# Kernel tuning notes

Measured on AMD Instinct MI355X. Metric: run time of the kernel, lower is better.

The kernel has to match this reference:

```python
import jax, jax.numpy as jnp
import numpy as np

B, C, H, W = 2, 256, 64, 64
NH, HD, K = 4, 64, 16  # num_head, head_channel, n_clusters
N = H * W
SCALE = HD ** 0.5


def _lin(x, Wm, b):
    return x @ Wm + b


def _mlp(x, W1, b1, W2, b2):
    h = _lin(x, W1, b1)
    h = jnp.where(h > 0, h, 0.01 * h)  # LeakyReLU(0.01)
    return _lin(h, W2, b2)  # dropout p=0.0 -> identity


def setup_inputs() -> dict:
    key = jax.random.key(0)
    ks = jax.random.split(key, 20)
    s = 1.0 / np.sqrt(C)
    s2 = 1.0 / np.sqrt(2 * C)
    inp = {
        "q_img": jax.random.normal(ks[0], (B, C, H, W), jnp.float32),
        "k_img_map": jax.random.normal(ks[1], (B, C, H, W), jnp.float32),
        "v_img_map": jax.random.normal(ks[2], (B, C, H, W), jnp.float32),
        "labels": jax.random.randint(ks[3], (B, H, W), 0, K),
        "pixel_coefficients": jax.random.uniform(ks[4], (B, N, N), jnp.float32),
        "Wq": jax.random.uniform(ks[5], (C, C), jnp.float32, -s, s),
        "bq": jnp.zeros((C,), jnp.float32),
        "Wk": jax.random.uniform(ks[6], (C, C), jnp.float32, -s, s),
        "bk": jnp.zeros((C,), jnp.float32),
        "Wv": jax.random.uniform(ks[7], (C, C), jnp.float32, -s, s),
        "bv": jnp.zeros((C,), jnp.float32),
        "W11": jax.random.uniform(ks[8], (C, 2 * C), jnp.float32, -s, s),
        "b11": jnp.zeros((2 * C,), jnp.float32),
        "W12": jax.random.uniform(ks[9], (2 * C, C), jnp.float32, -s2, s2),
        "b12": jnp.zeros((C,), jnp.float32),
        "W21": jax.random.uniform(ks[10], (C, 2 * C), jnp.float32, -s, s),
        "b21": jnp.zeros((2 * C,), jnp.float32),
        "W22": jax.random.uniform(ks[11], (2 * C, C), jnp.float32, -s2, s2),
        "b22": jnp.zeros((C,), jnp.float32),
    }
    return inp


def reference(q_img, k_img_map, v_img_map, labels, pixel_coefficients,
              Wq, bq, Wk, bk, Wv, bv, W11, b11, W12, b12, W21, b21, W22, b22):
    # [B,C,H,W] -> [B,N,C]
    q = _lin(q_img.transpose(0, 2, 3, 1).reshape(B, N, C), Wq, bq)
    k = _lin(k_img_map.transpose(0, 2, 3, 1).reshape(B, N, C), Wk, bk)
    v = _lin(v_img_map.transpose(0, 2, 3, 1).reshape(B, N, C), Wv, bv)

    lab = labels.reshape(B, N)
    onehot = (lab[:, :, None] == jnp.arange(K)[None, None, :]).astype(jnp.float32)  # [B,N,K]
    num_k = jnp.einsum('bnk,bnc->bkc', onehot, k)
    den_k = onehot.sum(axis=1)[:, :, None] + 1e-6
    centers_k = num_k / den_k  # [B,K,C]

    qm = q.reshape(B, N, NH, HD).transpose(0, 2, 1, 3)  # [B,h,N,d]
    km = k.reshape(B, N, NH, HD).transpose(0, 2, 1, 3)
    vm = v.reshape(B, N, NH, HD).transpose(0, 2, 1, 3)
    cm = centers_k.reshape(B, K, NH, HD).transpose(0, 2, 1, 3)  # [B,h,K,d]

    attn_intra = jnp.einsum('bhnd,bhmd->bhnm', qm, km)          # [B,h,N,N]
    attn_centers = jnp.einsum('bhnd,bhkd->bhnk', qm, cm)        # [B,h,N,K]

    same = (lab[:, :, None] == lab[:, None, :])[:, None]        # [B,1,N,N]
    idx = jnp.broadcast_to(lab[:, None, None, :], (B, NH, N, N))
    attn_inter = jnp.take_along_axis(attn_centers, idx, axis=-1) * pixel_coefficients[:, None]

    scores = jnp.where(same, attn_intra, attn_inter) / SCALE
    attn = jax.nn.softmax(scores, axis=-1)
    out = jnp.einsum('bhnm,bhmd->bhnd', attn, vm).transpose(0, 2, 1, 3).reshape(B, N, C)

    rs1 = v + _mlp(out, W11, b11, W12, b12)        # [B,N,C] (v_spatial residual)
    rs2 = rs1 + _mlp(rs1, W21, b21, W22, b22)
    return rs2.reshape(B, H, W, C).transpose(0, 3, 1, 2)  # [B,C,H,W]
```

## Files before the change

kernel.cpp:

```cpp
#include <hip/hip_runtime.h>
#include <stdint.h>

#define Bv 2
#define Cv 256
#define Nv 4096
#define NHv 4
#define HDv 64
#define Kv 16


typedef __attribute__((ext_vector_type(8))) short bf16x8;
typedef __attribute__((ext_vector_type(4))) float f32x4;

__device__ __forceinline__ float bf2f(unsigned short u) {
  union { unsigned int i; float f; } x; x.i = ((unsigned int)u) << 16; return x.f;
}
__device__ __forceinline__ unsigned short f2bf(float f) {
  union { float f; unsigned int i; } x; x.f = f;
  unsigned int r = x.i + 0x7FFF + ((x.i >> 16) & 1);
  return (unsigned short)(r >> 16);
}

__global__ __launch_bounds__(256) void imgt_k(
    const float* __restrict__ qi, const float* __restrict__ ki,
    const float* __restrict__ vi, unsigned short* __restrict__ dst)
{
  const int z = blockIdx.z;
  const float* src = (z < 2 ? qi : (z < 4 ? ki : vi)) + (long long)(z & 1) * Cv * Nv;
  unsigned short* out = dst + (long long)z * Nv * Cv;
  __shared__ float t[32][33];
  const int x = threadIdx.x, y = threadIdx.y;
  const int n0 = blockIdx.x * 32, c0 = blockIdx.y * 32;
  for (int i = y; i < 32; i += 8)
    t[i][x] = src[(long long)(c0 + i) * Nv + n0 + x];
  __syncthreads();
  for (int i = y; i < 32; i += 8)
    out[(long long)(n0 + i) * Cv + c0 + x] = f2bf(t[x][i]);
}

struct WP { const float* p[7]; };

__global__ __launch_bounds__(256) void wt_k(WP wp, unsigned short* __restrict__ dst)
{
  const int z = blockIdx.z;
  const int KD[7] = {256, 256, 256, 256, 512, 256, 512};
  const int ND[7] = {256, 256, 256, 512, 256, 512, 256};
  const long long OFF[7] = {0, 65536, 131072, 196608, 327680, 458752, 589824};
  const int Kw = KD[z], Nw = ND[z];
  const int nb = blockIdx.x * 32, kb2 = blockIdx.y * 32;
  if (nb >= Nw || kb2 >= Kw) return;
  __shared__ float t[32][33];
  const int x = threadIdx.x, y = threadIdx.y;
  const float* src = wp.p[z];
  for (int i = y; i < 32; i += 8)
    t[i][x] = src[(long long)(kb2 + i) * Nw + nb + x];
  __syncthreads();
  for (int i = y; i < 32; i += 8)
    dst[OFF[z] + (long long)(nb + i) * Kw + kb2 + x] = f2bf(t[x][i]);
}

__global__ __launch_bounds__(256) void proj_k(
    const unsigned short* __restrict__ imgT, const unsigned short* __restrict__ wt,
    const float* __restrict__ bq, const float* __restrict__ bk, const float* __restrict__ bv,
    unsigned short* __restrict__ qbf, unsigned short* __restrict__ kbf,
    float* __restrict__ vpp, unsigned short* __restrict__ vtb)
{
  __shared__ __align__(16) unsigned short As[128][72];
  __shared__ __align__(16) unsigned short Bs[128][72];
  const int tid = threadIdx.x;
  const int w = tid >> 6, lane = tid & 63;
  const int lr = lane & 15, quad = lane >> 4;
  const int m0 = blockIdx.x * 128, n0 = blockIdx.y * 128;
  const int z = blockIdx.z, zz = z >> 1, bb = z & 1;
  const int wm = (w >> 1) * 64, wn = (w & 1) * 64;
  const int sr = tid >> 1, sh = (tid & 1) * 32;
  const long long NvCv = (long long)Nv * Cv;

  const float* bias = zz == 0 ? bq : (zz == 1 ? bk : bv);
  const unsigned short* Ab0 = imgT + (long long)z * NvCv + (long long)(m0 + sr) * Cv + sh;
  const unsigned short* Bb0 = wt + (long long)zz * 65536 + (long long)(n0 + sr) * Cv + sh;

  f32x4 acc[4][4];
#pragma unroll
  for (int i = 0; i < 4; ++i)
#pragma unroll
    for (int j = 0; j < 4; ++j) acc[i][j] = (f32x4){0.f, 0.f, 0.f, 0.f};

  for (int k0 = 0; k0 < Cv; k0 += 64) {
    const unsigned short* Ab = Ab0 + k0;
    const unsigned short* Bp = Bb0 + k0;
    uint4 a0 = *(const uint4*)Ab, a1 = *(const uint4*)(Ab + 8);
    uint4 a2 = *(const uint4*)(Ab + 16), a3 = *(const uint4*)(Ab + 24);
    uint4 b0 = *(const uint4*)Bp, b1 = *(const uint4*)(Bp + 8);
    uint4 b2 = *(const uint4*)(Bp + 16), b3 = *(const uint4*)(Bp + 24);
    *(uint4*)&As[sr][sh] = a0; *(uint4*)&As[sr][sh + 8] = a1;
    *(uint4*)&As[sr][sh + 16] = a2; *(uint4*)&As[sr][sh + 24] = a3;
    *(uint4*)&Bs[sr][sh] = b0; *(uint4*)&Bs[sr][sh + 8] = b1;
    *(uint4*)&Bs[sr][sh + 16] = b2; *(uint4*)&Bs[sr][sh + 24] = b3;
    __syncthreads();
#pragma unroll
    for (int ks = 0; ks < 2; ++ks) {
      bf16x8 af[4], bfr[4];
#pragma unroll
      for (int i = 0; i < 4; ++i)
        af[i] = *(const bf16x8*)&As[wm + i * 16 + lr][ks * 32 + quad * 8];
#pragma unroll
      for (int j = 0; j < 4; ++j)
        bfr[j] = *(const bf16x8*)&Bs[wn + j * 16 + lr][ks * 32 + quad * 8];
#pragma unroll
      for (int i = 0; i < 4; ++i)
#pragma unroll
        for (int j = 0; j < 4; ++j)
          acc[i][j] = __builtin_amdgcn_mfma_f32_16x16x32_bf16(af[i], bfr[j], acc[i][j], 0, 0, 0);
    }
    __syncthreads();
  }

#pragma unroll
  for (int j = 0; j < 4; ++j) {
    const int col = n0 + wn + j * 16 + lr;
    const float bvv = bias[col];
#pragma unroll
    for (int i = 0; i < 4; ++i) {
      const int mb = m0 + wm + i * 16 + quad * 4;
      float r[4];
#pragma unroll
      for (int reg = 0; reg < 4; ++reg) r[reg] = acc[i][j][reg] + bvv;
      const long long ob = (long long)bb * NvCv;
      if (zz == 0) {
#pragma unroll
        for (int reg = 0; reg < 4; ++reg)
          qbf[ob + (long long)(mb + reg) * Cv + col] = f2bf(r[reg] * 0.125f);
      } else if (zz == 1) {
#pragma unroll
        for (int reg = 0; reg < 4; ++reg)
          kbf[ob + (long long)(mb + reg) * Cv + col] = f2bf(r[reg]);
      } else {
#pragma unroll
        for (int reg = 0; reg < 4; ++reg)
          vpp[ob + (long long)(mb + reg) * Cv + col] = r[reg];
        uint2 pk;
        pk.x = f2bf(r[0]) | ((unsigned int)f2bf(r[1]) << 16);
        pk.y = f2bf(r[2]) | ((unsigned int)f2bf(r[3]) << 16);
        *(uint2*)&vtb[ob + (long long)col * Nv + mb] = pk;
      }
    }
  }
}

template<bool ABF16, int ACT, int RES, int OM>
__global__ __launch_bounds__(256) void mm_k(
    const void* __restrict__ A, const unsigned short* __restrict__ Bt,
    const float* __restrict__ bias, const float* __restrict__ Res,
    float* __restrict__ outF, unsigned short* __restrict__ outB,
    int M, int Nn, int Kd)
{
  __shared__ __align__(16) unsigned short As[128][72];
  __shared__ __align__(16) unsigned short Bs[128][72];
  const int tid = threadIdx.x;
  const int w = tid >> 6, lane = tid & 63;
  const int lr = lane & 15, quad = lane >> 4;
  const int m0 = blockIdx.x * 128, n0 = blockIdx.y * 128;
  const int wm = (w >> 1) * 64, wn = (w & 1) * 64;
  const int sr = tid >> 1, sh = (tid & 1) * 32;

  f32x4 acc[4][4];
#pragma unroll
  for (int i = 0; i < 4; ++i)
#pragma unroll
    for (int j = 0; j < 4; ++j) acc[i][j] = (f32x4){0.f, 0.f, 0.f, 0.f};

  const long long abase = (long long)(m0 + sr) * Kd + sh;
  const unsigned short* Bb = Bt + (long long)(n0 + sr) * Kd + sh;

  for (int k0 = 0; k0 < Kd; k0 += 64) {
    if (ABF16) {
      const unsigned short* Ab = (const unsigned short*)A + abase + k0;
      uint4 u0 = *(const uint4*)Ab, u1 = *(const uint4*)(Ab + 8);
      uint4 u2 = *(const uint4*)(Ab + 16), u3 = *(const uint4*)(Ab + 24);
      *(uint4*)&As[sr][sh] = u0; *(uint4*)&As[sr][sh + 8] = u1;
      *(uint4*)&As[sr][sh + 16] = u2; *(uint4*)&As[sr][sh + 24] = u3;
    } else {
      const float* Af = (const float*)A + abase + k0;
#pragma unroll
      for (int t = 0; t < 4; ++t) {
        const float4 f0 = *(const float4*)(Af + t * 8);
        const float4 f1 = *(const float4*)(Af + t * 8 + 4);
        uint4 pk;
        pk.x = f2bf(f0.x) | ((unsigned int)f2bf(f0.y) << 16);
        pk.y = f2bf(f0.z) | ((unsigned int)f2bf(f0.w) << 16);
        pk.z = f2bf(f1.x) | ((unsigned int)f2bf(f1.y) << 16);
        pk.w = f2bf(f1.z) | ((unsigned int)f2bf(f1.w) << 16);
        *(uint4*)&As[sr][sh + t * 8] = pk;
      }
    }
    {
      const unsigned short* Bp = Bb + k0;
      uint4 u0 = *(const uint4*)Bp, u1 = *(const uint4*)(Bp + 8);
      uint4 u2 = *(const uint4*)(Bp + 16), u3 = *(const uint4*)(Bp + 24);
      *(uint4*)&Bs[sr][sh] = u0; *(uint4*)&Bs[sr][sh + 8] = u1;
      *(uint4*)&Bs[sr][sh + 16] = u2; *(uint4*)&Bs[sr][sh + 24] = u3;
    }
    __syncthreads();
#pragma unroll
    for (int ks = 0; ks < 2; ++ks) {
      bf16x8 af[4], bfr[4];
#pragma unroll
      for (int i = 0; i < 4; ++i)
        af[i] = *(const bf16x8*)&As[wm + i * 16 + lr][ks * 32 + quad * 8];
#pragma unroll
      for (int j = 0; j < 4; ++j)
        bfr[j] = *(const bf16x8*)&Bs[wn + j * 16 + lr][ks * 32 + quad * 8];
#pragma unroll
      for (int i = 0; i < 4; ++i)
#pragma unroll
        for (int j = 0; j < 4; ++j)
          acc[i][j] = __builtin_amdgcn_mfma_f32_16x16x32_bf16(af[i], bfr[j], acc[i][j], 0, 0, 0);
    }
    __syncthreads();
  }

#pragma unroll
  for (int j = 0; j < 4; ++j) {
    const int col = n0 + wn + j * 16 + lr;
    const float bv = bias[col];
#pragma unroll
    for (int i = 0; i < 4; ++i) {
      const int mb = m0 + wm + i * 16 + quad * 4;
      float r[4];
#pragma unroll
      for (int reg = 0; reg < 4; ++reg) {
        float v = acc[i][j][reg] + bv;
        if (ACT) v = v > 0.f ? v : 0.01f * v;
        if (RES) v += Res[(long long)(mb + reg) * Nn + col];
        r[reg] = v;
      }
      if (OM == 0) {
#pragma unroll
        for (int reg = 0; reg < 4; ++reg)
          outF[(long long)(mb + reg) * Nn + col] = r[reg];
      } else if (OM == 1) {
#pragma unroll
        for (int reg = 0; reg < 4; ++reg)
          outB[(long long)(mb + reg) * Nn + col] = f2bf(r[reg]);
      } else {
        const float4 st = {r[0], r[1], r[2], r[3]};
        *(float4*)&outF[((long long)((mb >> 12) * Cv + col)) * Nv + (mb & 4095)] = st;
      }
    }
  }
}

__global__ __launch_bounds__(256) void zero_k(float* p, int n)
{
  const int i = blockIdx.x * 256 + threadIdx.x;
  if (i < n) p[i] = 0.f;
}

__global__ __launch_bounds__(256) void center_accum(
    const unsigned short* __restrict__ kb, const int* __restrict__ labels,
    float* __restrict__ cent, float* __restrict__ cnts)
{
  __shared__ int lab_s[512];
  const int bx = blockIdx.x;
  const int chunk = bx & 7;
  const int kk = (bx >> 3) & 15;
  const int b = bx >> 7;
  const int c = threadIdx.x;
  const int nbase = chunk * 512;
  for (int i = threadIdx.x; i < 512; i += 256) lab_s[i] = labels[b * Nv + nbase + i];
  __syncthreads();
  float acc = 0.f;
  int cnt = 0;
#pragma unroll 4
  for (int i = 0; i < 512; ++i) {
    if (lab_s[i] == kk) {
      acc += bf2f(kb[(long long)(b * Nv + nbase + i) * Cv + c]);
      ++cnt;
    }
  }
  atomicAdd(&cent[(b * Kv + kk) * Cv + c], acc);
  if (c == 0) atomicAdd(&cnts[b * Kv + kk], (float)cnt);
}

__global__ __launch_bounds__(256) void center_norm(float* cent, const float* cnts)
{
  const int i = blockIdx.x * 256 + threadIdx.x;
  cent[i] = cent[i] / (cnts[i >> 8] + 1e-6f);
}

union PSCS {
  unsigned short p[4][16][68];
  float c[16][68];
};

__global__ __launch_bounds__(256) void attn_k(
    const unsigned short* __restrict__ qb, const unsigned short* __restrict__ kb,
    const unsigned short* __restrict__ vtb, const float* __restrict__ cent,
    const int* __restrict__ labels, const float* __restrict__ pc,
    float* __restrict__ opart, float* __restrict__ lpart)
{
  __shared__ __align__(16) unsigned short q_s[64][72];
  __shared__ __align__(16) unsigned short k_s[64][72];
  __shared__ __align__(16) unsigned short vt_s[64][72];
  __shared__ __align__(16) PSCS u_s;
  __shared__ float ac_s[64][17];

  const int tid = threadIdx.x;
  const int lane = tid & 63, w = tid >> 6;
  const int lr = lane & 15, quad = lane >> 4;
  const int bx = blockIdx.x;
  const int qt = bx & 63, h = (bx >> 6) & 3, b = (bx >> 8) & 1;
  const int part = bx >> 9;
  const int n0 = qt * 64;
  const int mbase = part * 2048;
  const int sr2 = tid >> 2, so2 = (tid & 3) * 16;
  const int row_l = w * 16 + quad * 4;
  const long long pcb = (long long)b * Nv * Nv;

  {
    const unsigned short* src = qb + ((long long)(b * Nv + n0 + sr2)) * Cv + h * HDv + so2;
    *(uint4*)&q_s[sr2][so2] = *(const uint4*)src;
    *(uint4*)&q_s[sr2][so2 + 8] = *(const uint4*)(src + 8);
  }
  for (int idx = tid; idx < Kv * HDv; idx += 256)
    u_s.c[idx >> 6][idx & 63] = cent[((long long)(b * Kv + (idx >> 6))) * Cv + h * HDv + (idx & 63)];

  uint4 ka0, ka1, va0, va1;
  float pc1[4][4];
  int labm1[4], labq[4];
  {
    const long long ks = ((long long)(b * Nv + mbase + sr2)) * Cv + h * HDv + so2;
    ka0 = *(const uint4*)(kb + ks); ka1 = *(const uint4*)(kb + ks + 8);
    const long long vs = ((long long)(b * Cv + h * HDv + sr2)) * Nv + mbase + so2;
    va0 = *(const uint4*)(vtb + vs); va1 = *(const uint4*)(vtb + vs + 8);
  }
#pragma unroll
  for (int sub = 0; sub < 4; ++sub) {
    labm1[sub] = labels[b * Nv + mbase + sub * 16 + lr];
#pragma unroll
    for (int reg = 0; reg < 4; ++reg)
      pc1[sub][reg] = pc[pcb + (long long)(n0 + row_l + reg) * Nv + mbase + sub * 16 + lr];
  }
#pragma unroll
  for (int reg = 0; reg < 4; ++reg) labq[reg] = labels[b * Nv + n0 + row_l + reg];

  __syncthreads();
  for (int idx = tid; idx < 64 * Kv; idx += 256) {
    const int r = idx >> 4, kk = idx & 15;
    float s = 0.f;
#pragma unroll
    for (int d = 0; d < HDv; ++d) s += bf2f(q_s[r][d]) * u_s.c[kk][d];
    ac_s[r][kk] = s;
  }
  const bf16x8 qa0 = *(const bf16x8*)&q_s[w * 16 + lr][quad * 8];
  const bf16x8 qa1 = *(const bf16x8*)&q_s[w * 16 + lr][32 + quad * 8];
  __syncthreads();

  *(uint4*)&k_s[sr2][so2] = ka0; *(uint4*)&k_s[sr2][so2 + 8] = ka1;
  *(uint4*)&vt_s[sr2][so2] = va0; *(uint4*)&vt_s[sr2][so2 + 8] = va1;
  __syncthreads();

  f32x4 oacc[4];
#pragma unroll
  for (int s2 = 0; s2 < 4; ++s2) oacc[s2] = (f32x4){0.f, 0.f, 0.f, 0.f};
  float lrow[4] = {0.f, 0.f, 0.f, 0.f};

  for (int t = 0; t < 32; ++t) {
    const int m0 = mbase + t * 64;
    const bool has = (t < 31);

    if (has) {
      const long long ks = ((long long)(b * Nv + m0 + 64 + sr2)) * Cv + h * HDv + so2;
      ka0 = *(const uint4*)(kb + ks); ka1 = *(const uint4*)(kb + ks + 8);
      const long long vs = ((long long)(b * Cv + h * HDv + sr2)) * Nv + m0 + 64 + so2;
      va0 = *(const uint4*)(vtb + vs); va1 = *(const uint4*)(vtb + vs + 8);
    }

    f32x4 sacc[4];
#pragma unroll
    for (int sub = 0; sub < 4; ++sub) {
      const bf16x8 kb0 = *(const bf16x8*)&k_s[sub * 16 + lr][quad * 8];
      const bf16x8 kb1 = *(const bf16x8*)&k_s[sub * 16 + lr][32 + quad * 8];
      f32x4 s = (f32x4){0.f, 0.f, 0.f, 0.f};
      s = __builtin_amdgcn_mfma_f32_16x16x32_bf16(qa0, kb0, s, 0, 0, 0);
      s = __builtin_amdgcn_mfma_f32_16x16x32_bf16(qa1, kb1, s, 0, 0, 0);
      sacc[sub] = s;
    }

#pragma unroll
    for (int reg = 0; reg < 4; ++reg) {
      const int Ln = labq[reg];
#pragma unroll
      for (int sub = 0; sub < 4; ++sub) {
        const float s = (labm1[sub] == Ln) ? sacc[sub][reg]
                                           : ac_s[row_l + reg][labm1[sub]] * pc1[sub][reg];
        const float p = __expf(s - 4.0f);
        lrow[reg] += p;
        u_s.p[w][quad * 4 + reg][sub * 16 + lr] = f2bf(p);
      }
    }

    if (has) {
#pragma unroll
      for (int sub = 0; sub < 4; ++sub) {
        labm1[sub] = labels[b * Nv + m0 + 64 + sub * 16 + lr];
#pragma unroll
        for (int reg = 0; reg < 4; ++reg)
          pc1[sub][reg] = pc[pcb + (long long)(n0 + row_l + reg) * Nv + m0 + 64 + sub * 16 + lr];
      }
    }

    const bf16x8 pa0 = *(const bf16x8*)&u_s.p[w][lr][quad * 8];
    const bf16x8 pa1 = *(const bf16x8*)&u_s.p[w][lr][32 + quad * 8];
#pragma unroll
    for (int sub = 0; sub < 4; ++sub) {
      const bf16x8 vb0 = *(const bf16x8*)&vt_s[sub * 16 + lr][quad * 8];
      const bf16x8 vb1 = *(const bf16x8*)&vt_s[sub * 16 + lr][32 + quad * 8];
      oacc[sub] = __builtin_amdgcn_mfma_f32_16x16x32_bf16(pa0, vb0, oacc[sub], 0, 0, 0);
      oacc[sub] = __builtin_amdgcn_mfma_f32_16x16x32_bf16(pa1, vb1, oacc[sub], 0, 0, 0);
    }

    __syncthreads();
    if (has) {
      *(uint4*)&k_s[sr2][so2] = ka0; *(uint4*)&k_s[sr2][so2 + 8] = ka1;
      *(uint4*)&vt_s[sr2][so2] = va0; *(uint4*)&vt_s[sr2][so2 + 8] = va1;
    }
    __syncthreads();
  }

#pragma unroll
  for (int reg = 0; reg < 4; ++reg) {
    float l = lrow[reg];
    l += __shfl_xor(l, 1); l += __shfl_xor(l, 2);
    l += __shfl_xor(l, 4); l += __shfl_xor(l, 8);
    const int row = n0 + row_l + reg;
    const long long obase = (long long)part * 2097152 + ((long long)(b * Nv + row)) * Cv + h * HDv;
#pragma unroll
    for (int sub = 0; sub < 4; ++sub)
      opart[obase + sub * 16 + lr] = oacc[sub][reg];
    if (lr == 0)
      lpart[part * 32768 + (b * 4 + h) * 4096 + row] = l;
  }
}

__global__ __launch_bounds__(256) void combine_k(
    const float* __restrict__ op, const float* __restrict__ lp,
    unsigned short* __restrict__ aob)
{
  const long long i4 = ((long long)blockIdx.x * 256 + threadIdx.x) * 4;
  const int c = (int)(i4 & 255), n = (int)((i4 >> 8) & 4095), b = (int)(i4 >> 20);
  const int h = c >> 6;
  const float l = lp[(b * 4 + h) * 4096 + n] + lp[32768 + (b * 4 + h) * 4096 + n];
  const float inv = 1.f / l;
  const float4 a = *(const float4*)&op[i4];
  const float4 d = *(const float4*)&op[2097152 + i4];
  uint2 pk;
  pk.x = f2bf((a.x + d.x) * inv) | ((unsigned int)f2bf((a.y + d.y) * inv) << 16);
  pk.y = f2bf((a.z + d.z) * inv) | ((unsigned int)f2bf((a.w + d.w) * inv) << 16);
  *(uint2*)&aob[i4] = pk;
}

extern "C" void kernel_launch(void* const* d_in, const int* in_sizes, int n_in,
                              void* d_out, int out_size, void* d_ws, size_t ws_size,
                              hipStream_t stream)
{
  const float* q_img = (const float*)d_in[0];
  const float* k_img = (const float*)d_in[1];
  const float* v_img = (const float*)d_in[2];
  const int* labels  = (const int*)d_in[3];
  const float* pc    = (const float*)d_in[4];
  const float* Wq  = (const float*)d_in[5];  const float* bq  = (const float*)d_in[6];
  const float* Wk  = (const float*)d_in[7];  const float* bk  = (const float*)d_in[8];
  const float* Wv  = (const float*)d_in[9];  const float* bv  = (const float*)d_in[10];
  const float* W11 = (const float*)d_in[11]; const float* b11 = (const float*)d_in[12];
  const float* W12 = (const float*)d_in[13]; const float* b12 = (const float*)d_in[14];
  const float* W21 = (const float*)d_in[15]; const float* b21 = (const float*)d_in[16];
  const float* W22 = (const float*)d_in[17]; const float* b22 = (const float*)d_in[18];
  float* outp = (float*)d_out;

  const long long SZ = (long long)Bv * Nv * Cv;
  float* ws    = (float*)d_ws;
  float* vpp   = ws;
  float* rs1   = vpp + SZ;
  float* opart = rs1 + SZ;
  float* lpart = opart + 2 * SZ;
  float* cent  = lpart + 65536;
  float* cnts  = cent + Bv * Kv * Cv;
  unsigned short* wt   = (unsigned short*)(cnts + Bv * Kv);
  unsigned short* qbf  = wt + 720896;
  unsigned short* kbf  = qbf + SZ;
  unsigned short* vtb  = kbf + SZ;
  unsigned short* aob  = vtb + SZ;
  unsigned short* h1b  = aob + SZ;
  unsigned short* imgT = aob;

  imgt_k<<<dim3(Nv / 32, Cv / 32, 6), dim3(32, 8), 0, stream>>>(q_img, k_img, v_img, imgT);
  WP wp = {{Wq, Wk, Wv, W11, W12, W21, W22}};
  wt_k<<<dim3(16, 16, 7), dim3(32, 8), 0, stream>>>(wp, wt);

  proj_k<<<dim3(32, 2, 6), 256, 0, stream>>>(imgT, wt, bq, bk, bv, qbf, kbf, vpp, vtb);

  zero_k<<<dim3(33), 256, 0, stream>>>(cent, Bv * Kv * Cv + Bv * Kv);
  center_accum<<<dim3(Bv * Kv * 8), 256, 0, stream>>>(kbf, labels, cent, cnts);
  center_norm<<<dim3(Bv * Kv * Cv / 256), 256, 0, stream>>>(cent, cnts);

  attn_k<<<dim3(1024), 256, 0, stream>>>(qbf, kbf, vtb, cent, labels, pc, opart, lpart);
  combine_k<<<dim3(2048), 256, 0, stream>>>(opart, lpart, aob);

  mm_k<true, 1, 0, 1><<<dim3(64, 4), 256, 0, stream>>>(
      aob, wt + 196608, b11, nullptr, nullptr, h1b, 2 * Nv, 2 * Cv, Cv);
  mm_k<true, 0, 1, 0><<<dim3(64, 2), 256, 0, stream>>>(
      h1b, wt + 327680, b12, vpp, rs1, nullptr, 2 * Nv, Cv, 2 * Cv);

  mm_k<false, 1, 0, 1><<<dim3(64, 4), 256, 0, stream>>>(
      rs1, wt + 458752, b21, nullptr, nullptr, h1b, 2 * Nv, 2 * Cv, Cv);
  mm_k<true, 0, 1, 4><<<dim3(64, 2), 256, 0, stream>>>(
      h1b, wt + 589824, b22, rs1, outp, nullptr, 2 * Nv, Cv, 2 * Cv);
}
```

Before: 447.9 us.

## Shrink MLP GEMM tiles, use exp2 softmax, packed bf16 converts and MFMA priority

The MLP GEMMs now use 64x64 tiles, giving four times as many blocks so more of the GPU's compute units are busy on these small matrices. In attention, the Q scale now folds in log2(e) so the kernel can call the hardware exp2 (v_exp_f32) directly in place of __expf. The fixed -4 max offset is dropped, which raises the risk of overflow. Center-score gathers are hoisted into registers and prefetched for the next tile, P is packed with v_cvt_pk_bf16, and MFMA sections are wrapped in s_setprio. Other bf16 stores in the V projection and the combine kernel also use the packed convert.

```diff
diff --git a/kernel.cpp b/kernel.cpp
--- a/kernel.cpp
+++ b/kernel.cpp
@@ -19,6 +19,16 @@
   union { float f; unsigned int i; } x; x.f = f;
   unsigned int r = x.i + 0x7FFF + ((x.i >> 16) & 1);
   return (unsigned short)(r >> 16);
+}
+__device__ __forceinline__ unsigned int cvt_pk_bf16(float lo, float hi) {
+  unsigned int r;
+  asm("v_cvt_pk_bf16_f32 %0, %1, %2" : "=v"(r) : "v"(lo), "v"(hi));
+  return r;
+}
+__device__ __forceinline__ float exp2_raw(float x) {
+  float r;
+  asm("v_exp_f32 %0, %1" : "=v"(r) : "v"(x));
+  return r;
 }
 
 __global__ __launch_bounds__(256) void imgt_k(
@@ -130,7 +140,7 @@
       if (zz == 0) {
 #pragma unroll
         for (int reg = 0; reg < 4; ++reg)
-          qbf[ob + (long long)(mb + reg) * Cv + col] = f2bf(r[reg] * 0.125f);
+          qbf[ob + (long long)(mb + reg) * Cv + col] = f2bf(r[reg] * 0.18033688f);
       } else if (zz == 1) {
 #pragma unroll
         for (int reg = 0; reg < 4; ++reg)
@@ -140,8 +150,8 @@
         for (int reg = 0; reg < 4; ++reg)
           vpp[ob + (long long)(mb + reg) * Cv + col] = r[reg];
         uint2 pk;
-        pk.x = f2bf(r[0]) | ((unsigned int)f2bf(r[1]) << 16);
-        pk.y = f2bf(r[2]) | ((unsigned int)f2bf(r[3]) << 16);
+        pk.x = cvt_pk_bf16(r[0], r[1]);
+        pk.y = cvt_pk_bf16(r[2], r[3]);
         *(uint2*)&vtb[ob + (long long)col * Nv + mb] = pk;
       }
     }
@@ -149,26 +159,26 @@
 }
 
 template<bool ABF16, int ACT, int RES, int OM>
-__global__ __launch_bounds__(256) void mm_k(
+__global__ __launch_bounds__(256) void mm64_k(
     const void* __restrict__ A, const unsigned short* __restrict__ Bt,
     const float* __restrict__ bias, const float* __restrict__ Res,
     float* __restrict__ outF, unsigned short* __restrict__ outB,
     int M, int Nn, int Kd)
 {
-  __shared__ __align__(16) unsigned short As[128][72];
-  __shared__ __align__(16) unsigned short Bs[128][72];
+  __shared__ __align__(16) unsigned short As[64][72];
+  __shared__ __align__(16) unsigned short Bs[64][72];
   const int tid = threadIdx.x;
   const int w = tid >> 6, lane = tid & 63;
   const int lr = lane & 15, quad = lane >> 4;
-  const int m0 = blockIdx.x * 128, n0 = blockIdx.y * 128;
-  const int wm = (w >> 1) * 64, wn = (w & 1) * 64;
-  const int sr = tid >> 1, sh = (tid & 1) * 32;
-
-  f32x4 acc[4][4];
-#pragma unroll
-  for (int i = 0; i < 4; ++i)
-#pragma unroll
-    for (int j = 0; j < 4; ++j) acc[i][j] = (f32x4){0.f, 0.f, 0.f, 0.f};
+  const int m0 = blockIdx.x * 64, n0 = blockIdx.y * 64;
+  const int wm = (w >> 1) * 32, wn = (w & 1) * 32;
+  const int sr = tid >> 2, sh = (tid & 3) * 16;
+
+  f32x4 acc[2][2];
+#pragma unroll
+  for (int i = 0; i < 2; ++i)
+#pragma unroll
+    for (int j = 0; j < 2; ++j) acc[i][j] = (f32x4){0.f, 0.f, 0.f, 0.f};
 
   const long long abase = (long long)(m0 + sr) * Kd + sh;
   const unsigned short* Bb = Bt + (long long)(n0 + sr) * Kd + sh;
@@ -177,13 +187,11 @@
     if (ABF16) {
       const unsigned short* Ab = (const unsigned short*)A + abase + k0;
       uint4 u0 = *(const uint4*)Ab, u1 = *(const uint4*)(Ab + 8);
-      uint4 u2 = *(const uint4*)(Ab + 16), u3 = *(const uint4*)(Ab + 24);
       *(uint4*)&As[sr][sh] = u0; *(uint4*)&As[sr][sh + 8] = u1;
-      *(uint4*)&As[sr][sh + 16] = u2; *(uint4*)&As[sr][sh + 24] = u3;
     } else {
       const float* Af = (const float*)A + abase + k0;
 #pragma unroll
-      for (int t = 0; t < 4; ++t) {
+      for (int t = 0; t < 2; ++t) {
         const float4 f0 = *(const float4*)(Af + t * 8);
         const float4 f1 = *(const float4*)(Af + t * 8 + 4);
         uint4 pk;
@@ -197,35 +205,33 @@
     {
       const unsigned short* Bp = Bb + k0;
       uint4 u0 = *(const uint4*)Bp, u1 = *(const uint4*)(Bp + 8);
-      uint4 u2 = *(const uint4*)(Bp + 16), u3 = *(const uint4*)(Bp + 24);
       *(uint4*)&Bs[sr][sh] = u0; *(uint4*)&Bs[sr][sh + 8] = u1;
-      *(uint4*)&Bs[sr][sh + 16] = u2; *(uint4*)&Bs[sr][sh + 24] = u3;
     }
     __syncthreads();
 #pragma unroll
     for (int ks = 0; ks < 2; ++ks) {
-      bf16x8 af[4], bfr[4];
-#pragma unroll
-      for (int i = 0; i < 4; ++i)
+      bf16x8 af[2], bfr[2];
+#pragma unroll
+      for (int i = 0; i < 2; ++i)
         af[i] = *(const bf16x8*)&As[wm + i * 16 + lr][ks * 32 + quad * 8];
 #pragma unroll
-      for (int j = 0; j < 4; ++j)
+      for (int j = 0; j < 2; ++j)
         bfr[j] = *(const bf16x8*)&Bs[wn + j * 16 + lr][ks * 32 + quad * 8];
 #pragma unroll
-      for (int i = 0; i < 4; ++i)
-#pragma unroll
-        for (int j = 0; j < 4; ++j)
+      for (int i = 0; i < 2; ++i)
+#pragma unroll
+        for (int j = 0; j < 2; ++j)
           acc[i][j] = __builtin_amdgcn_mfma_f32_16x16x32_bf16(af[i], bfr[j], acc[i][j], 0, 0, 0);
     }
     __syncthreads();
   }
 
 #pragma unroll
-  for (int j = 0; j < 4; ++j) {
+  for (int j = 0; j < 2; ++j) {
     const int col = n0 + wn + j * 16 + lr;
     const float bv = bias[col];
 #pragma unroll
-    for (int i = 0; i < 4; ++i) {
+    for (int i = 0; i < 2; ++i) {
       const int mb = m0 + wm + i * 16 + quad * 4;
       float r[4];
 #pragma unroll
@@ -357,6 +363,13 @@
   const bf16x8 qa1 = *(const bf16x8*)&q_s[w * 16 + lr][32 + quad * 8];
   __syncthreads();
 
+  float acg[4][4];
+#pragma unroll
+  for (int sub = 0; sub < 4; ++sub)
+#pragma unroll
+    for (int reg = 0; reg < 4; ++reg)
+      acg[sub][reg] = ac_s[row_l + reg][labm1[sub]];
+
   *(uint4*)&k_s[sr2][so2] = ka0; *(uint4*)&k_s[sr2][so2 + 8] = ka1;
   *(uint4*)&vt_s[sr2][so2] = va0; *(uint4*)&vt_s[sr2][so2 + 8] = va1;
   __syncthreads();
@@ -378,6 +391,7 @@
     }
 
     f32x4 sacc[4];
+    __builtin_amdgcn_s_setprio(1);
 #pragma unroll
     for (int sub = 0; sub < 4; ++sub) {
       const bf16x8 kb0 = *(const bf16x8*)&k_s[sub * 16 + lr][quad * 8];
@@ -387,18 +401,26 @@
       s = __builtin_amdgcn_mfma_f32_16x16x32_bf16(qa1, kb1, s, 0, 0, 0);
       sacc[sub] = s;
     }
-
-#pragma unroll
-    for (int reg = 0; reg < 4; ++reg) {
-      const int Ln = labq[reg];
-#pragma unroll
-      for (int sub = 0; sub < 4; ++sub) {
-        const float s = (labm1[sub] == Ln) ? sacc[sub][reg]
-                                           : ac_s[row_l + reg][labm1[sub]] * pc1[sub][reg];
-        const float p = __expf(s - 4.0f);
+    __builtin_amdgcn_s_setprio(0);
+
+#pragma unroll
+    for (int sub = 0; sub < 4; ++sub) {
+      float p4[4];
+#pragma unroll
+      for (int reg = 0; reg < 4; ++reg) {
+        const float s = (labm1[sub] == labq[reg]) ? sacc[sub][reg]
+                                                  : acg[sub][reg] * pc1[sub][reg];
+        const float p = exp2_raw(s);
         lrow[reg] += p;
-        u_s.p[w][quad * 4 + reg][sub * 16 + lr] = f2bf(p);
+        p4[reg] = p;
       }
+      const unsigned int pk01 = cvt_pk_bf16(p4[0], p4[1]);
+      const unsigned int pk23 = cvt_pk_bf16(p4[2], p4[3]);
+      unsigned short* pp = &u_s.p[w][quad * 4][sub * 16 + lr];
+      pp[0]   = (unsigned short)pk01;
+      pp[68]  = (unsigned short)(pk01 >> 16);
+      pp[136] = (unsigned short)pk23;
+      pp[204] = (unsigned short)(pk23 >> 16);
     }
 
     if (has) {
@@ -413,12 +435,22 @@
 
     const bf16x8 pa0 = *(const bf16x8*)&u_s.p[w][lr][quad * 8];
     const bf16x8 pa1 = *(const bf16x8*)&u_s.p[w][lr][32 + quad * 8];
+    __builtin_amdgcn_s_setprio(1);
 #pragma unroll
     for (int sub = 0; sub < 4; ++sub) {
       const bf16x8 vb0 = *(const bf16x8*)&vt_s[sub * 16 + lr][quad * 8];
       const bf16x8 vb1 = *(const bf16x8*)&vt_s[sub * 16 + lr][32 + quad * 8];
       oacc[sub] = __builtin_amdgcn_mfma_f32_16x16x32_bf16(pa0, vb0, oacc[sub], 0, 0, 0);
       oacc[sub] = __builtin_amdgcn_mfma_f32_16x16x32_bf16(pa1, vb1, oacc[sub], 0, 0, 0);
+    }
+    __builtin_amdgcn_s_setprio(0);
+
+    if (has) {
+#pragma unroll
+      for (int sub = 0; sub < 4; ++sub)
+#pragma unroll
+        for (int reg = 0; reg < 4; ++reg)
+          acg[sub][reg] = ac_s[row_l + reg][labm1[sub]];
     }
 
     __syncthreads();
@@ -456,8 +488,8 @@
   const float4 a = *(const float4*)&op[i4];
   const float4 d = *(const float4*)&op[2097152 + i4];
   uint2 pk;
-  pk.x = f2bf((a.x + d.x) * inv) | ((unsigned int)f2bf((a.y + d.y) * inv) << 16);
-  pk.y = f2bf((a.z + d.z) * inv) | ((unsigned int)f2bf((a.w + d.w) * inv) << 16);
+  pk.x = cvt_pk_bf16((a.x + d.x) * inv, (a.y + d.y) * inv);
+  pk.y = cvt_pk_bf16((a.z + d.z) * inv, (a.w + d.w) * inv);
   *(uint2*)&aob[i4] = pk;
 }
 
@@ -508,13 +540,13 @@
   attn_k<<<dim3(1024), 256, 0, stream>>>(qbf, kbf, vtb, cent, labels, pc, opart, lpart);
   combine_k<<<dim3(2048), 256, 0, stream>>>(opart, lpart, aob);
 
-  mm_k<true, 1, 0, 1><<<dim3(64, 4), 256, 0, stream>>>(
+  mm64_k<true, 1, 0, 1><<<dim3(128, 8), 256, 0, stream>>>(
       aob, wt + 196608, b11, nullptr, nullptr, h1b, 2 * Nv, 2 * Cv, Cv);
-  mm_k<true, 0, 1, 0><<<dim3(64, 2), 256, 0, stream>>>(
+  mm64_k<true, 0, 1, 0><<<dim3(128, 4), 256, 0, stream>>>(
       h1b, wt + 327680, b12, vpp, rs1, nullptr, 2 * Nv, Cv, 2 * Cv);
 
-  mm_k<false, 1, 0, 1><<<dim3(64, 4), 256, 0, stream>>>(
+  mm64_k<false, 1, 0, 1><<<dim3(128, 8), 256, 0, stream>>>(
       rs1, wt + 458752, b21, nullptr, nullptr, h1b, 2 * Nv, 2 * Cv, Cv);
-  mm_k<true, 0, 1, 4><<<dim3(64, 2), 256, 0, stream>>>(
+  mm64_k<true, 0, 1, 4><<<dim3(128, 4), 256, 0, stream>>>(
       h1b, wt + 589824, b22, rs1, outp, nullptr, 2 * Nv, Cv, 2 * Cv);
 }
```

Result: faster. 408.3 us (-8.8%).
